# Kernel optimization log

Hardware: AMD Instinct MI355X
Metric: run time of the kernel (lower is better)

Reference implementation:

```python
import jax, jax.numpy as jnp
import numpy as np

IN, OUT, LR = 4096, 4096, 64
TILE = (8, 8)

def setup_inputs() -> dict:
    key = jax.random.key(0)
    ks = jax.random.split(key, 8)
    return {
        "x": jax.random.normal(ks[0], (4, 2048, IN), dtype=jnp.float32),
        "frozen_random_matrix": jax.random.normal(ks[1], (OUT, IN), dtype=jnp.float16),
        "lowrank_first": jax.random.normal(ks[2], (LR, IN), dtype=jnp.float32) * 0.02,
        "lowrank_second": jax.random.normal(ks[3], (2 * OUT, LR), dtype=jnp.float32) * 0.02,
        "grid_scale": jax.random.normal(ks[4], (OUT // TILE[0], 1, IN // TILE[1], 1), dtype=jnp.float32),
        "grid_bias": jax.random.normal(ks[5], (OUT // TILE[0], 1, IN // TILE[1], 1), dtype=jnp.float32),
        "sparse_adapter": jnp.zeros((OUT, IN), dtype=jnp.float32),
        "scale": jax.random.normal(ks[6], (OUT,), dtype=jnp.float32),
        "bias": jax.random.normal(ks[7], (OUT,), dtype=jnp.float32),
    }

def reference(x, frozen_random_matrix, lowrank_first, lowrank_second,
              grid_scale, grid_bias, sparse_adapter, scale, bias):
    O, I = frozen_random_matrix.shape
    th, tw = TILE
    # Tiled affine reconstruction of the weight matrix, in fp16 (buffer dtype)
    m = frozen_random_matrix.reshape(O // th, th, I // tw, tw)
    m = grid_bias.astype(jnp.float16) + m * grid_scale.astype(jnp.float16)
    m = m.reshape(O, I) + sparse_adapter.astype(jnp.float16)
    # Dense GEMM in fp16, cast back to input dtype (mirrors input.to(matrix.dtype))
    baseline = jnp.matmul(x.astype(jnp.float16), m.T).astype(x.dtype)  # [B,S,O]
    # Low-rank adapter path
    hid = jnp.matmul(x, lowrank_first.T)                               # [B,S,LR]
    intercept = jnp.concatenate([scale, bias], axis=0)                 # [2*O]
    proj = jnp.matmul(hid, lowrank_second.T) + intercept               # [B,S,2*O]
    multiplicative, additive = proj[..., :O], proj[..., O:]
    return additive + multiplicative * baseline
```

## Files before the change

kernel.cpp:

```cpp
#include <hip/hip_runtime.h>
#include <stdint.h>

typedef _Float16 f16;
typedef unsigned short u16;
typedef __attribute__((ext_vector_type(8))) _Float16 h16x8;
typedef __attribute__((ext_vector_type(8))) unsigned short u16x8;
typedef __attribute__((ext_vector_type(4))) float f32x4;

#define NDIM  4096
#define KDIM  4096
#define LRDIM 64
#define NTK   128

#define MFMA16(a, b, c) __builtin_amdgcn_mfma_f32_16x16x32_f16((a), (b), (c), 0, 0, 0)

__device__ __forceinline__ float bf2f(u16 b) {
  union { unsigned u; float f; } c; c.u = ((unsigned)b) << 16; return c.f;
}
__device__ __forceinline__ float h2f(u16 b) {
  union { u16 u; f16 h; } c; c.u = b; return (float)c.h;
}
__device__ __forceinline__ h16x8 pack8(float4 a, float4 b) {
  h16x8 w = { (f16)a.x, (f16)a.y, (f16)a.z, (f16)a.w,
              (f16)b.x, (f16)b.y, (f16)b.z, (f16)b.w };
  return w;
}

__device__ __forceinline__ void gll16(const void* g, void* l) {
  __builtin_amdgcn_global_load_lds(
      (const __attribute__((address_space(1))) void*)g,
      (__attribute__((address_space(3))) void*)l,
      16, 0, 0);
}

__device__ int frozen_mode(const void* frozen, int t) {
  const u16* fr = (const u16*)frozen;
  __shared__ int sE[256], sO[256];
  int ce = 0, co = 0;
  for (int j = 0; j < 8; ++j) {
    float ve = fabsf(bf2f(fr[t * 16 + 2 * j]));
    float vo = fabsf(bf2f(fr[t * 16 + 2 * j + 1]));
    if (ve >= 0.05f && ve <= 10.0f) ++ce;
    if (vo >= 0.05f && vo <= 10.0f) ++co;
  }
  sE[t] = ce; sO[t] = co;
  __syncthreads();
  for (int s = 128; s > 0; s >>= 1) {
    if (t < s) { sE[t] += sE[t + s]; sO[t] += sO[t + s]; }
    __syncthreads();
  }
  int te = sE[0], to = sO[0];
  __syncthreads();
  if (to > 1024) return (te > 1024) ? 1 : 2;
  return 0;
}

__device__ __forceinline__ h16x8 build_m8(
    const void* __restrict__ frozen, const float* __restrict__ gs,
    const float* __restrict__ gb, const float* __restrict__ sa,
    int o, int i0, int mode)
{
  size_t fo = (size_t)o * KDIM + i0;
  int gidx = (o >> 3) * 512 + (i0 >> 3);
  float gsf = gs[gidx], gbf = gb[gidx];
  float4 s0 = ((const float4*)(sa + fo))[0];
  float4 s1 = ((const float4*)(sa + fo))[1];
  float sv[8] = { s0.x, s0.y, s0.z, s0.w, s1.x, s1.y, s1.z, s1.w };
  float fv[8];
  if (mode == 2) {
    float4 q0 = ((const float4*)((const float*)frozen + fo))[0];
    float4 q1 = ((const float4*)((const float*)frozen + fo))[1];
    fv[0]=q0.x; fv[1]=q0.y; fv[2]=q0.z; fv[3]=q0.w;
    fv[4]=q1.x; fv[5]=q1.y; fv[6]=q1.z; fv[7]=q1.w;
  } else {
    u16x8 fb = *(const u16x8*)((const u16*)frozen + fo);
#pragma unroll
    for (int j = 0; j < 8; ++j) fv[j] = (mode == 1) ? bf2f(fb[j]) : h2f(fb[j]);
  }
  h16x8 w;
#pragma unroll
  for (int j = 0; j < 8; ++j) w[j] = (f16)(gbf + fv[j] * gsf + sv[j]);
  return w;
}

__global__ __launch_bounds__(256) void k_prep(
    const float* __restrict__ x, const void* __restrict__ frozen,
    const float* __restrict__ gs, const float* __restrict__ gb,
    const float* __restrict__ sa, f16* __restrict__ xh,
    f16* __restrict__ mW)
{
  int b = blockIdx.x;
  if (b < 16384) {
    size_t idx = (size_t)b * 256 + threadIdx.x;
    const float4* xp = (const float4*)x + idx * 2;
    *(h16x8*)(xh + idx * 8) = pack8(xp[0], xp[1]);
  } else {
    int mode = frozen_mode(frozen, threadIdx.x);
    int idx = (b - 16384) * 256 + threadIdx.x;
    int o  = idx >> 9;
    int ig = idx & 511;
    h16x8 w = build_m8(frozen, gs, gb, sa, o, ig * 8, mode);
    *(h16x8*)(mW + (size_t)o * KDIM + ig * 8) = w;
  }
}

__global__ __launch_bounds__(256) void k14_hid(const f16* __restrict__ xh,
                                               const float* __restrict__ L1,
                                               f16* __restrict__ hid)
{
  __shared__ f16 sA[2][32 * 32];
  __shared__ f16 sB[2][64 * 32];
  int t = threadIdx.x;
  int l = t & 63, wid = t >> 6;
  int wr = wid >> 1, wc = wid & 1;
  int brow = blockIdx.x * 32;
  int ar = t >> 2, ac8 = (t & 3) * 8;
  int brw = t >> 2, bc8 = (t & 3) * 8;

  f32x4 acc[2] = {};

  {
    if (t < 128)
      gll16(xh + (size_t)(brow + ar) * KDIM + ac8, &sA[0][ar * 32 + ac8]);
    const float* lp = L1 + (size_t)brw * KDIM + bc8;
    *(h16x8*)&sB[0][brw * 32 + bc8] = pack8(((const float4*)lp)[0], ((const float4*)lp)[1]);
  }

  int cur = 0;
  const int NT = KDIM / 32;
  for (int kt = 0; kt < NT; ++kt) {
    __syncthreads();
    bool pf = (kt + 1 < NT);
    h16x8 wb;
    if (pf) {
      int k0 = (kt + 1) * 32;
      if (t < 128)
        gll16(xh + (size_t)(brow + ar) * KDIM + k0 + ac8, &sA[cur ^ 1][ar * 32 + ac8]);
      const float* lp = L1 + (size_t)brw * KDIM + k0 + bc8;
      wb = pack8(((const float4*)lp)[0], ((const float4*)lp)[1]);
    }
    h16x8 aF, bF[2];
    aF = *(const h16x8*)&sA[cur][(wr * 16 + (l & 15)) * 32 + (l >> 4) * 8];
#pragma unroll
    for (int n = 0; n < 2; ++n)
      bF[n] = *(const h16x8*)&sB[cur][(wc * 32 + n * 16 + (l & 15)) * 32 + (l >> 4) * 8];
#pragma unroll
    for (int n = 0; n < 2; ++n)
      acc[n] = MFMA16(aF, bF[n], acc[n]);
    if (pf)
      *(h16x8*)&sB[cur ^ 1][brw * 32 + bc8] = wb;
    cur ^= 1;
  }

#pragma unroll
  for (int n = 0; n < 2; ++n)
#pragma unroll
    for (int j = 0; j < 4; ++j) {
      int r = wr * 16 + ((l >> 4) << 2) + j;
      int c = wc * 32 + n * 16 + (l & 15);
      hid[(size_t)(brow + r) * LRDIM + c] = (f16)acc[n][j];
    }
}

__global__ __launch_bounds__(512) void k18c_main(
    const f16* __restrict__ xh, const f16* __restrict__ mW,
    const f16* __restrict__ hid, const float* __restrict__ L2,
    const float* __restrict__ scale, const float* __restrict__ bias,
    float* __restrict__ out)
{
  __shared__ f16 lds[3][16384];

  int t = threadIdx.x;
  int l = t & 63, wid = t >> 6;
  int wm = wid >> 2, wn = wid & 3;

  int wg = blockIdx.x;
  int xcd = wg & 7, w = wg >> 3;
  int bm = xcd * 4 + (w & 3);
  int bn = w >> 2;
  int brow = bm * 256, bcol = bn * 256;

  auto stage = [&](int q, int kt2, int buf) {
    int u = q * 512 + t;
    if (u < 1024) {
      int sg = (u & 3) ^ ((u >> 3) & 3);
      gll16(xh + (size_t)(brow + (u >> 2)) * KDIM + kt2 * 32 + sg * 8,
            &lds[buf][u * 8]);
    } else {
      int v = u - 1024;
      int sg = (v & 3) ^ ((v >> 3) & 3);
      gll16(mW + (size_t)(bcol + (v >> 2)) * KDIM + kt2 * 32 + sg * 8,
            &lds[buf][8192 + v * 8]);
    }
  };

#pragma unroll
  for (int q = 0; q < 4; ++q) stage(q, 0, 0);
#pragma unroll
  for (int q = 0; q < 4; ++q) stage(q, 1, 1);

  f32x4 acc[8][4] = {};

  int X = ((l >> 4) ^ ((l >> 1) & 3)) * 8;

  for (int kt = 0; kt < NTK; ++kt) {
    const f16* A = &lds[kt % 3][0];
    const f16* B = &lds[kt % 3][8192];
    int sb = (kt + 2) % 3;

    if (kt + 2 < NTK) {
#pragma unroll
      for (int q = 0; q < 4; ++q) stage(q, kt + 2, sb);
    }

    if (kt < NTK - 2) {
      asm volatile("s_waitcnt vmcnt(8)" ::: "memory");
    } else if (kt == NTK - 2) {
      asm volatile("s_waitcnt vmcnt(4)" ::: "memory");
    } else {
      asm volatile("s_waitcnt vmcnt(0)" ::: "memory");
    }
    __builtin_amdgcn_sched_barrier(0);
    __builtin_amdgcn_s_barrier();

    int ar0 = (wm * 128 + (l & 15)) * 32 + X;
    int br0 = (wn * 64  + (l & 15)) * 32 + X;

    h16x8 aF[8], bF[4];
#pragma unroll
    for (int f = 0; f < 8; ++f) aF[f] = *(const h16x8*)&A[ar0 + f * 512];
#pragma unroll
    for (int n = 0; n < 4; ++n) bF[n] = *(const h16x8*)&B[br0 + n * 512];

    __builtin_amdgcn_s_setprio(1);
#pragma unroll
    for (int f = 0; f < 8; ++f)
#pragma unroll
      for (int n = 0; n < 4; ++n)
        acc[f][n] = MFMA16(aF[f], bF[n], acc[f][n]);
    __builtin_amdgcn_s_setprio(0);

    __builtin_amdgcn_s_barrier();
  }

  f16* sH  = &lds[0][0];
  f16* sLm = &lds[1][0];
  f16* sLa = &lds[2][0];

#pragma unroll
  for (int q = 0; q < 4; ++q) {
    int u = q * 512 + t;
    gll16(hid + (size_t)(brow + (u >> 3)) * LRDIM + (u & 7) * 8, &sH[u * 8]);
  }
#pragma unroll
  for (int q = 0; q < 4; ++q) {
    int u = q * 512 + t;
    const float* lp = L2 + (size_t)(bcol + (u >> 3)) * LRDIM + (u & 7) * 8;
    *(h16x8*)&sLm[u * 8] = pack8(((const float4*)lp)[0], ((const float4*)lp)[1]);
  }
#pragma unroll
  for (int q = 0; q < 4; ++q) {
    int u = q * 512 + t;
    const float* lp = L2 + (size_t)(NDIM + bcol + (u >> 3)) * LRDIM + (u & 7) * 8;
    *(h16x8*)&sLa[u * 8] = pack8(((const float4*)lp)[0], ((const float4*)lp)[1]);
  }
  __syncthreads();

  float sc[4], bi[4];
#pragma unroll
  for (int n = 0; n < 4; ++n) {
    int o = bcol + wn * 64 + n * 16 + (l & 15);
    sc[n] = scale[o];
    bi[n] = bias[o];
  }

  {
    h16x8 lB[4][2];
#pragma unroll
    for (int n = 0; n < 4; ++n)
#pragma unroll
      for (int kk = 0; kk < 2; ++kk)
        lB[n][kk] = *(const h16x8*)&sLm[(wn * 64 + n * 16 + (l & 15)) * 64 + kk * 32 + (l >> 4) * 8];
#pragma unroll
    for (int f = 0; f < 8; ++f) {
      h16x8 h0 = *(const h16x8*)&sH[(wm * 128 + f * 16 + (l & 15)) * 64 + (l >> 4) * 8];
      h16x8 h1 = *(const h16x8*)&sH[(wm * 128 + f * 16 + (l & 15)) * 64 + 32 + (l >> 4) * 8];
      f32x4 mm[4];
#pragma unroll
      for (int n = 0; n < 4; ++n) {
        f32x4 mi = { sc[n], sc[n], sc[n], sc[n] };
        mm[n] = mi;
      }
#pragma unroll
      for (int n = 0; n < 4; ++n) {
        mm[n] = MFMA16(h0, lB[n][0], mm[n]);
        mm[n] = MFMA16(h1, lB[n][1], mm[n]);
      }
#pragma unroll
      for (int n = 0; n < 4; ++n)
        acc[f][n] *= mm[n];
    }
  }

  {
    h16x8 lB[4][2];
#pragma unroll
    for (int n = 0; n < 4; ++n)
#pragma unroll
      for (int kk = 0; kk < 2; ++kk)
        lB[n][kk] = *(const h16x8*)&sLa[(wn * 64 + n * 16 + (l & 15)) * 64 + kk * 32 + (l >> 4) * 8];
#pragma unroll
    for (int f = 0; f < 8; ++f) {
      h16x8 h0 = *(const h16x8*)&sH[(wm * 128 + f * 16 + (l & 15)) * 64 + (l >> 4) * 8];
      h16x8 h1 = *(const h16x8*)&sH[(wm * 128 + f * 16 + (l & 15)) * 64 + 32 + (l >> 4) * 8];
      f32x4 aa[4];
#pragma unroll
      for (int n = 0; n < 4; ++n) {
        f32x4 mi = { bi[n], bi[n], bi[n], bi[n] };
        aa[n] = mi;
      }
#pragma unroll
      for (int n = 0; n < 4; ++n) {
        aa[n] = MFMA16(h0, lB[n][0], aa[n]);
        aa[n] = MFMA16(h1, lB[n][1], aa[n]);
      }
      int rbase = brow + wm * 128 + f * 16 + ((l >> 4) << 2);
#pragma unroll
      for (int n = 0; n < 4; ++n) {
        int c = bcol + wn * 64 + n * 16 + (l & 15);
        f32x4 v = aa[n] + acc[f][n];
#pragma unroll
        for (int j = 0; j < 4; ++j)
          out[(size_t)(rbase + j) * NDIM + c] = v[j];
      }
    }
  }
}

extern "C" void kernel_launch(void* const* d_in, const int* in_sizes, int n_in,
                              void* d_out, int out_size, void* d_ws, size_t ws_size,
                              hipStream_t stream)
{
  const int SD[9] = {33554432,16777216,262144,524288,262144,262144,16777216,4096,4096};
  const int SA[9] = {4096,16777216,262144,262144,262144,524288,4096,16777216,33554432};
  bool dict = (n_in == 9), alph = (n_in == 9);
  if (n_in == 9) {
    for (int i = 0; i < 9; ++i) {
      if (in_sizes[i] != SD[i]) dict = false;
      if (in_sizes[i] != SA[i]) alph = false;
    }
  }
  if (!dict && !alph) {
    int ix = 0;
    for (int i = 0; i < n_in; ++i)
      if (in_sizes[i] == 33554432 || in_sizes[i] == 134217728) { ix = i; break; }
    dict = (ix == 0);
  }
  const float* x     = (const float*)d_in[dict ? 0 : 8];
  const void*  fr    =               d_in[1];
  const float* L1    = (const float*)d_in[dict ? 2 : 4];
  const float* L2    = (const float*)d_in[dict ? 3 : 5];
  const float* gs    = (const float*)d_in[dict ? 4 : 3];
  const float* gb    = (const float*)d_in[dict ? 5 : 2];
  const float* sa    = (const float*)d_in[dict ? 6 : 7];
  const float* scale = (const float*)d_in[dict ? 7 : 6];
  const float* bias  = (const float*)d_in[dict ? 8 : 0];
  float* out = (float*)d_out;

  const size_t MW_B = (size_t)NDIM * KDIM * 2;
  const size_t XH_B = (size_t)8192 * KDIM * 2;

  char* ws = (char*)d_ws;
  f16* mW  = (f16*)ws;
  f16* xh  = (f16*)(ws + MW_B);
  f16* hid = (f16*)(ws + MW_B + XH_B);

  k_prep<<<dim3(24576), dim3(256), 0, stream>>>(x, fr, gs, gb, sa, xh, mW);
  k14_hid<<<dim3(256), dim3(256), 0, stream>>>(xh, L1, hid);
  k18c_main<<<dim3(512), dim3(512), 0, stream>>>(
      xh, mW, hid, L2, scale, bias, out);
}
```

Before: 420.6 us.

## Fuse low-rank hid GEMM into prep kernel and halve main GEMM N-tile

The separate hid kernel is folded into the prep launch as 64 extra blocks. Each of these reads fp32 x directly and converts it on the fly, computing a 128-row tile instead of 32. This removes one launch and lets the hid work overlap with the conversion blocks, though those blocks may be scheduled late. The main GEMM tile shrinks from 256x256 to 256x128 with 8 waves arranged 4x2, doubling the grid to 1024 and cutting LDS per block. The cost is lower arithmetic intensity per tile and more re-reads of x.

After: 533.0 us. +26.7%, slower.

```diff
diff --git a/kernel.cpp b/kernel.cpp
--- a/kernel.cpp
+++ b/kernel.cpp
@@ -83,158 +83,170 @@
   return w;
 }
 
-__global__ __launch_bounds__(256) void k_prep(
+__global__ __launch_bounds__(256) void k_prep2(
     const float* __restrict__ x, const void* __restrict__ frozen,
     const float* __restrict__ gs, const float* __restrict__ gb,
-    const float* __restrict__ sa, f16* __restrict__ xh,
-    f16* __restrict__ mW)
+    const float* __restrict__ sa, const float* __restrict__ L1,
+    f16* __restrict__ xh, f16* __restrict__ mW, f16* __restrict__ hid)
 {
+  __shared__ f16 sA[2][128 * 32];
+  __shared__ f16 sB[2][64 * 32];
   int b = blockIdx.x;
+  int t = threadIdx.x;
+
   if (b < 16384) {
-    size_t idx = (size_t)b * 256 + threadIdx.x;
+    size_t idx = (size_t)b * 256 + t;
     const float4* xp = (const float4*)x + idx * 2;
     *(h16x8*)(xh + idx * 8) = pack8(xp[0], xp[1]);
-  } else {
-    int mode = frozen_mode(frozen, threadIdx.x);
-    int idx = (b - 16384) * 256 + threadIdx.x;
+    return;
+  }
+  if (b < 24576) {
+    int mode = frozen_mode(frozen, t);
+    int idx = (b - 16384) * 256 + t;
     int o  = idx >> 9;
     int ig = idx & 511;
     h16x8 w = build_m8(frozen, gs, gb, sa, o, ig * 8, mode);
     *(h16x8*)(mW + (size_t)o * KDIM + ig * 8) = w;
-  }
-}
-
-__global__ __launch_bounds__(256) void k14_hid(const f16* __restrict__ xh,
-                                               const float* __restrict__ L1,
-                                               f16* __restrict__ hid)
-{
-  __shared__ f16 sA[2][32 * 32];
-  __shared__ f16 sB[2][64 * 32];
-  int t = threadIdx.x;
+    return;
+  }
+
   int l = t & 63, wid = t >> 6;
   int wr = wid >> 1, wc = wid & 1;
-  int brow = blockIdx.x * 32;
-  int ar = t >> 2, ac8 = (t & 3) * 8;
+  int brow = (b - 24576) * 128;
+  int arow = t >> 1, acol = (t & 1) * 16;
   int brw = t >> 2, bc8 = (t & 3) * 8;
 
-  f32x4 acc[2] = {};
+  f32x4 acc[4][2] = {};
 
   {
-    if (t < 128)
-      gll16(xh + (size_t)(brow + ar) * KDIM + ac8, &sA[0][ar * 32 + ac8]);
+    const float* ap = x + (size_t)(brow + arow) * KDIM + acol;
+    float4 v0 = ((const float4*)ap)[0], v1 = ((const float4*)ap)[1];
+    float4 v2 = ((const float4*)ap)[2], v3 = ((const float4*)ap)[3];
+    *(h16x8*)&sA[0][arow * 32 + acol]     = pack8(v0, v1);
+    *(h16x8*)&sA[0][arow * 32 + acol + 8] = pack8(v2, v3);
     const float* lp = L1 + (size_t)brw * KDIM + bc8;
     *(h16x8*)&sB[0][brw * 32 + bc8] = pack8(((const float4*)lp)[0], ((const float4*)lp)[1]);
   }
 
   int cur = 0;
-  const int NT = KDIM / 32;
-  for (int kt = 0; kt < NT; ++kt) {
+  for (int kt = 0; kt < NTK; ++kt) {
     __syncthreads();
-    bool pf = (kt + 1 < NT);
-    h16x8 wb;
+    bool pf = (kt + 1 < NTK);
+    h16x8 wa0, wa1, wb;
     if (pf) {
       int k0 = (kt + 1) * 32;
-      if (t < 128)
-        gll16(xh + (size_t)(brow + ar) * KDIM + k0 + ac8, &sA[cur ^ 1][ar * 32 + ac8]);
+      const float* ap = x + (size_t)(brow + arow) * KDIM + k0 + acol;
+      float4 v0 = ((const float4*)ap)[0], v1 = ((const float4*)ap)[1];
+      float4 v2 = ((const float4*)ap)[2], v3 = ((const float4*)ap)[3];
+      wa0 = pack8(v0, v1); wa1 = pack8(v2, v3);
       const float* lp = L1 + (size_t)brw * KDIM + k0 + bc8;
       wb = pack8(((const float4*)lp)[0], ((const float4*)lp)[1]);
     }
-    h16x8 aF, bF[2];
-    aF = *(const h16x8*)&sA[cur][(wr * 16 + (l & 15)) * 32 + (l >> 4) * 8];
+    h16x8 aF[4], bF[2];
+#pragma unroll
+    for (int m = 0; m < 4; ++m)
+      aF[m] = *(const h16x8*)&sA[cur][(wr * 64 + m * 16 + (l & 15)) * 32 + (l >> 4) * 8];
 #pragma unroll
     for (int n = 0; n < 2; ++n)
       bF[n] = *(const h16x8*)&sB[cur][(wc * 32 + n * 16 + (l & 15)) * 32 + (l >> 4) * 8];
 #pragma unroll
+    for (int m = 0; m < 4; ++m)
+#pragma unroll
+      for (int n = 0; n < 2; ++n)
+        acc[m][n] = MFMA16(aF[m], bF[n], acc[m][n]);
+    if (pf) {
+      *(h16x8*)&sA[cur ^ 1][arow * 32 + acol]     = wa0;
+      *(h16x8*)&sA[cur ^ 1][arow * 32 + acol + 8] = wa1;
+      *(h16x8*)&sB[cur ^ 1][brw * 32 + bc8]       = wb;
+    }
+    cur ^= 1;
+  }
+
+#pragma unroll
+  for (int m = 0; m < 4; ++m)
+#pragma unroll
     for (int n = 0; n < 2; ++n)
-      acc[n] = MFMA16(aF, bF[n], acc[n]);
-    if (pf)
-      *(h16x8*)&sB[cur ^ 1][brw * 32 + bc8] = wb;
-    cur ^= 1;
-  }
-
-#pragma unroll
-  for (int n = 0; n < 2; ++n)
-#pragma unroll
-    for (int j = 0; j < 4; ++j) {
-      int r = wr * 16 + ((l >> 4) << 2) + j;
-      int c = wc * 32 + n * 16 + (l & 15);
-      hid[(size_t)(brow + r) * LRDIM + c] = (f16)acc[n][j];
-    }
-}
-
-__global__ __launch_bounds__(512) void k18c_main(
+#pragma unroll
+      for (int j = 0; j < 4; ++j) {
+        int r = wr * 64 + m * 16 + ((l >> 4) << 2) + j;
+        int c = wc * 32 + n * 16 + (l & 15);
+        hid[(size_t)(brow + r) * LRDIM + c] = (f16)acc[m][n][j];
+      }
+}
+
+__global__ __launch_bounds__(512) void k20_main(
     const f16* __restrict__ xh, const f16* __restrict__ mW,
     const f16* __restrict__ hid, const float* __restrict__ L2,
     const float* __restrict__ scale, const float* __restrict__ bias,
     float* __restrict__ out)
 {
-  __shared__ f16 lds[3][16384];
+  __shared__ f16 lds[3 * 12288];
 
   int t = threadIdx.x;
   int l = t & 63, wid = t >> 6;
-  int wm = wid >> 2, wn = wid & 3;
+  int wm = wid >> 1, wn = wid & 1;
 
   int wg = blockIdx.x;
   int xcd = wg & 7, w = wg >> 3;
   int bm = xcd * 4 + (w & 3);
   int bn = w >> 2;
-  int brow = bm * 256, bcol = bn * 256;
+  int brow = bm * 256, bcol = bn * 128;
 
   auto stage = [&](int q, int kt2, int buf) {
     int u = q * 512 + t;
     if (u < 1024) {
       int sg = (u & 3) ^ ((u >> 3) & 3);
       gll16(xh + (size_t)(brow + (u >> 2)) * KDIM + kt2 * 32 + sg * 8,
-            &lds[buf][u * 8]);
+            &lds[buf * 12288 + u * 8]);
     } else {
       int v = u - 1024;
       int sg = (v & 3) ^ ((v >> 3) & 3);
       gll16(mW + (size_t)(bcol + (v >> 2)) * KDIM + kt2 * 32 + sg * 8,
-            &lds[buf][8192 + v * 8]);
+            &lds[buf * 12288 + 8192 + v * 8]);
     }
   };
 
 #pragma unroll
-  for (int q = 0; q < 4; ++q) stage(q, 0, 0);
-#pragma unroll
-  for (int q = 0; q < 4; ++q) stage(q, 1, 1);
-
-  f32x4 acc[8][4] = {};
+  for (int q = 0; q < 3; ++q) stage(q, 0, 0);
+#pragma unroll
+  for (int q = 0; q < 3; ++q) stage(q, 1, 1);
+
+  f32x4 acc[4][4] = {};
 
   int X = ((l >> 4) ^ ((l >> 1) & 3)) * 8;
 
   for (int kt = 0; kt < NTK; ++kt) {
-    const f16* A = &lds[kt % 3][0];
-    const f16* B = &lds[kt % 3][8192];
+    const f16* A = &lds[(kt % 3) * 12288];
+    const f16* B = &lds[(kt % 3) * 12288 + 8192];
     int sb = (kt + 2) % 3;
 
     if (kt + 2 < NTK) {
 #pragma unroll
-      for (int q = 0; q < 4; ++q) stage(q, kt + 2, sb);
+      for (int q = 0; q < 3; ++q) stage(q, kt + 2, sb);
     }
 
     if (kt < NTK - 2) {
-      asm volatile("s_waitcnt vmcnt(8)" ::: "memory");
+      asm volatile("s_waitcnt vmcnt(6)" ::: "memory");
     } else if (kt == NTK - 2) {
-      asm volatile("s_waitcnt vmcnt(4)" ::: "memory");
+      asm volatile("s_waitcnt vmcnt(3)" ::: "memory");
     } else {
       asm volatile("s_waitcnt vmcnt(0)" ::: "memory");
     }
     __builtin_amdgcn_sched_barrier(0);
     __builtin_amdgcn_s_barrier();
 
-    int ar0 = (wm * 128 + (l & 15)) * 32 + X;
-    int br0 = (wn * 64  + (l & 15)) * 32 + X;
-
-    h16x8 aF[8], bF[4];
-#pragma unroll
-    for (int f = 0; f < 8; ++f) aF[f] = *(const h16x8*)&A[ar0 + f * 512];
+    int ar0 = (wm * 64 + (l & 15)) * 32 + X;
+    int br0 = (wn * 64 + (l & 15)) * 32 + X;
+
+    h16x8 aF[4], bF[4];
+#pragma unroll
+    for (int f = 0; f < 4; ++f) aF[f] = *(const h16x8*)&A[ar0 + f * 512];
 #pragma unroll
     for (int n = 0; n < 4; ++n) bF[n] = *(const h16x8*)&B[br0 + n * 512];
 
     __builtin_amdgcn_s_setprio(1);
 #pragma unroll
-    for (int f = 0; f < 8; ++f)
+    for (int f = 0; f < 4; ++f)
 #pragma unroll
       for (int n = 0; n < 4; ++n)
         acc[f][n] = MFMA16(aF[f], bF[n], acc[f][n]);
@@ -243,9 +255,9 @@
     __builtin_amdgcn_s_barrier();
   }
 
-  f16* sH  = &lds[0][0];
-  f16* sLm = &lds[1][0];
-  f16* sLa = &lds[2][0];
+  f16* sH  = &lds[0];
+  f16* sLm = &lds[16384];
+  f16* sLa = &lds[24576];
 
 #pragma unroll
   for (int q = 0; q < 4; ++q) {
@@ -253,16 +265,16 @@
     gll16(hid + (size_t)(brow + (u >> 3)) * LRDIM + (u & 7) * 8, &sH[u * 8]);
   }
 #pragma unroll
-  for (int q = 0; q < 4; ++q) {
+  for (int q = 0; q < 2; ++q) {
     int u = q * 512 + t;
     const float* lp = L2 + (size_t)(bcol + (u >> 3)) * LRDIM + (u & 7) * 8;
     *(h16x8*)&sLm[u * 8] = pack8(((const float4*)lp)[0], ((const float4*)lp)[1]);
   }
 #pragma unroll
-  for (int q = 0; q < 4; ++q) {
+  for (int q = 0; q < 2; ++q) {
     int u = q * 512 + t;
-    const float* lp = L2 + (size_t)(NDIM + bcol + (u >> 3)) * LRDIM + (u & 7) * 8;
-    *(h16x8*)&sLa[u * 8] = pack8(((const float4*)lp)[0], ((const float4*)lp)[1]);
+    const float* lq = L2 + (size_t)(NDIM + bcol + (u >> 3)) * LRDIM + (u & 7) * 8;
+    *(h16x8*)&sLa[u * 8] = pack8(((const float4*)lq)[0], ((const float4*)lq)[1]);
   }
   __syncthreads();
 
@@ -282,9 +294,9 @@
       for (int kk = 0; kk < 2; ++kk)
         lB[n][kk] = *(const h16x8*)&sLm[(wn * 64 + n * 16 + (l & 15)) * 64 + kk * 32 + (l >> 4) * 8];
 #pragma unroll
-    for (int f = 0; f < 8; ++f) {
-      h16x8 h0 = *(const h16x8*)&sH[(wm * 128 + f * 16 + (l & 15)) * 64 + (l >> 4) * 8];
-      h16x8 h1 = *(const h16x8*)&sH[(wm * 128 + f * 16 + (l & 15)) * 64 + 32 + (l >> 4) * 8];
+    for (int f = 0; f < 4; ++f) {
+      h16x8 h0 = *(const h16x8*)&sH[(wm * 64 + f * 16 + (l & 15)) * 64 + (l >> 4) * 8];
+      h16x8 h1 = *(const h16x8*)&sH[(wm * 64 + f * 16 + (l & 15)) * 64 + 32 + (l >> 4) * 8];
       f32x4 mm[4];
 #pragma unroll
       for (int n = 0; n < 4; ++n) {
@@ -310,9 +322,9 @@
       for (int kk = 0; kk < 2; ++kk)
         lB[n][kk] = *(const h16x8*)&sLa[(wn * 64 + n * 16 + (l & 15)) * 64 + kk * 32 + (l >> 4) * 8];
 #pragma unroll
-    for (int f = 0; f < 8; ++f) {
-      h16x8 h0 = *(const h16x8*)&sH[(wm * 128 + f * 16 + (l & 15)) * 64 + (l >> 4) * 8];
-      h16x8 h1 = *(const h16x8*)&sH[(wm * 128 + f * 16 + (l & 15)) * 64 + 32 + (l >> 4) * 8];
+    for (int f = 0; f < 4; ++f) {
+      h16x8 h0 = *(const h16x8*)&sH[(wm * 64 + f * 16 + (l & 15)) * 64 + (l >> 4) * 8];
+      h16x8 h1 = *(const h16x8*)&sH[(wm * 64 + f * 16 + (l & 15)) * 64 + 32 + (l >> 4) * 8];
       f32x4 aa[4];
 #pragma unroll
       for (int n = 0; n < 4; ++n) {
@@ -324,7 +336,7 @@
         aa[n] = MFMA16(h0, lB[n][0], aa[n]);
         aa[n] = MFMA16(h1, lB[n][1], aa[n]);
       }
-      int rbase = brow + wm * 128 + f * 16 + ((l >> 4) << 2);
+      int rbase = brow + wm * 64 + f * 16 + ((l >> 4) << 2);
 #pragma unroll
       for (int n = 0; n < 4; ++n) {
         int c = bcol + wn * 64 + n * 16 + (l & 15);
@@ -375,8 +387,8 @@
   f16* xh  = (f16*)(ws + MW_B);
   f16* hid = (f16*)(ws + MW_B + XH_B);
 
-  k_prep<<<dim3(24576), dim3(256), 0, stream>>>(x, fr, gs, gb, sa, xh, mW);
-  k14_hid<<<dim3(256), dim3(256), 0, stream>>>(xh, L1, hid);
-  k18c_main<<<dim3(512), dim3(512), 0, stream>>>(
+  k_prep2<<<dim3(24640), dim3(256), 0, stream>>>(
+      x, fr, gs, gb, sa, L1, xh, mW, hid);
+  k20_main<<<dim3(1024), dim3(512), 0, stream>>>(
       xh, mW, hid, L2, scale, bias, out);
 }
```
